# Kernel optimization log

Hardware: AMD Instinct MI355X
Metric: run time of the kernel (lower is better)

Reference implementation:

```python
import math
import jax, jax.numpy as jnp
import numpy as np

SINKHORN_ITERS = 5
SINKHORN_REG = 1.0
D_MODEL, KDIM, VDIM = 512, 512, 512
B, T, N = 8, 2048, 2048


def _xavier(key, shape):
    fan_in, fan_out = shape[0], shape[1]
    bound = math.sqrt(6.0 / (fan_in + fan_out))
    return jax.random.uniform(key, shape, jnp.float32, -bound, bound)


def setup_inputs() -> dict:
    key = jax.random.key(0)
    kq, kk, kv, kQ, kK, kV = jax.random.split(key, 6)
    return {
        "q": jax.random.normal(kq, (T, D_MODEL), jnp.float32),
        "k": jax.random.normal(kk, (B, N, KDIM), jnp.float32),
        "v": jax.random.normal(kv, (B, N, VDIM), jnp.float32),
        "Q": _xavier(kQ, (D_MODEL, D_MODEL)),
        "K": _xavier(kK, (KDIM, D_MODEL)),
        "V": _xavier(kV, (VDIM, D_MODEL)),
    }


def _cdist(q, k):
    # q: [T, d], k: [B, N, d] -> Euclidean distances [B, T, N]
    q2 = jnp.sum(q * q, axis=-1)            # [T]
    k2 = jnp.sum(k * k, axis=-1)            # [B, N]
    qk = jnp.einsum('td,bnd->btn', q, k)    # [B, T, N]
    sq = q2[None, :, None] + k2[:, None, :] - 2.0 * qk
    return jnp.sqrt(jnp.maximum(sq, 0.0))


def _sinkhorn(q, k, iters, reg):
    costs = _cdist(q, k)                    # [B, T, N]
    Kmat = -costs / reg
    num_params = k.shape[1]
    num_tokens = q.shape[0]
    log_a = -jnp.log(jnp.float32(num_params))
    log_b = jnp.float32(0.0)
    u = jnp.zeros((k.shape[0], 1, num_params), Kmat.dtype)
    v = jnp.zeros((k.shape[0], num_tokens, 1), Kmat.dtype)
    for _ in range(iters):
        u = log_a - jax.scipy.special.logsumexp(Kmat + v, axis=1, keepdims=True)
        v = log_b - jax.scipy.special.logsumexp(Kmat + u, axis=2, keepdims=True)
    return jnp.exp(Kmat + u + v)


def reference(q, k, v, Q, K, V):
    qp = q @ Q                               # [T, d_model]
    kp = k @ K                               # [B, N, d_model]
    vp = v @ V                               # [B, N, d_model]
    pi = _sinkhorn(qp, kp, SINKHORN_ITERS, SINKHORN_REG)  # [B, T, N]
    return jnp.einsum('btn,bnd->btd', pi, vp)              # [B, T, d_model]
```

## Files before the change

kernel.cpp:

```cpp
#include <hip/hip_runtime.h>
#include <math.h>

#define TT 2048
#define NP 2048
#define BB 8
#define DD 512

#define LOG_A (-7.6246189861593985f)
#define CC 30.0f
#define E30 1.0686475e13f
#define K0U 5.2180055e9f

typedef __attribute__((ext_vector_type(8))) _Float16 f16x8;
typedef __attribute__((ext_vector_type(4))) _Float16 f16x4;
typedef __attribute__((ext_vector_type(4))) float f32x4;

#define MFMA_F16(a, b, c)  __builtin_amdgcn_mfma_f32_16x16x32_f16((a), (b), (c), 0, 0, 0)

__device__ __forceinline__ float f16u2f(unsigned short u) {
    union { unsigned short s; _Float16 h; } v; v.s = u;
    return (float)v.h;
}

__device__ __forceinline__ void gload16(const void* g, void* l) {
    __builtin_amdgcn_global_load_lds(
        (const __attribute__((address_space(1))) void*)g,
        (__attribute__((address_space(3))) void*)l, 16, 0, 0);
}

__device__ __forceinline__ void frag_step_f16(
    const _Float16* sA, const _Float16* sB,
    int lane, int wm, int wn, f32x4 acc[4][4])
{
    const int sb = (lane >> 4) << 11;
    const int rl = (lane & 15) << 4;
    f16x8 a[4], b[4];
    #pragma unroll
    for (int i = 0; i < 4; ++i) {
        a[i] = *(const f16x8*)((const char*)sA + sb + ((wm + i * 16) << 4) + rl);
        b[i] = *(const f16x8*)((const char*)sB + sb + ((wn + i * 16) << 4) + rl);
    }
    #pragma unroll
    for (int i = 0; i < 4; ++i)
        #pragma unroll
        for (int j = 0; j < 4; ++j)
            acc[i][j] = MFMA_F16(a[i], b[j], acc[i][j]);
}

__device__ __forceinline__ void zero_acc(f32x4 acc[4][4]) {
    #pragma unroll
    for (int i = 0; i < 4; ++i)
        #pragma unroll
        for (int j = 0; j < 4; ++j)
            acc[i][j] = (f32x4){0.f, 0.f, 0.f, 0.f};
}

__device__ __forceinline__ void store_plain(
    float* C, int N, int row0, int col0, int lane, int wm, int wn, f32x4 acc[4][4])
{
    #pragma unroll
    for (int i = 0; i < 4; ++i)
        #pragma unroll
        for (int j = 0; j < 4; ++j) {
            int colg = col0 + wn + j * 16 + (lane & 15);
            int rowb = row0 + wm + i * 16 + ((lane >> 4) << 2);
            #pragma unroll
            for (int r = 0; r < 4; ++r)
                C[(size_t)(rowb + r) * N + colg] = acc[i][j][r];
        }
}

__global__ __launch_bounds__(256) void transpose_f16(
    const float* __restrict__ X, _Float16* __restrict__ oT, int R, int C)
{
    const size_t zoff = (size_t)blockIdx.z * R * C;
    const float* Xb = X + zoff;
    _Float16* ob = oT + zoff;
    __shared__ float t[64][65];
    const int bx = blockIdx.x * 64;
    const int by = blockIdx.y * 64;
    const int tx = threadIdx.x & 63, ty = threadIdx.x >> 6;
    #pragma unroll
    for (int r = ty; r < 64; r += 4)
        t[r][tx] = Xb[(size_t)(by + r) * C + bx + tx];
    __syncthreads();
    #pragma unroll
    for (int r = ty; r < 64; r += 4)
        ob[(size_t)(bx + r) * R + by + tx] = (_Float16)t[tx][r];
}

template<int OUT>
__global__ __launch_bounds__(256) void gemm_proj_f16(
    const float* __restrict__ A, const _Float16* __restrict__ Bt,
    _Float16* __restrict__ C, int M, int N, int K)
{
    __shared__ __attribute__((aligned(16))) _Float16 sA[4096], sB[4096];
    const int tid = threadIdx.x;
    const int lane = tid & 63;
    const int row0 = blockIdx.y * 128;
    const int col0 = blockIdx.x * 128;
    const int wm = ((tid >> 7) & 1) * 64;
    const int wn = ((tid >> 6) & 1) * 64;
    f32x4 acc[4][4];
    zero_acc(acc);

    for (int k0 = 0; k0 < K; k0 += 32) {
        __syncthreads();
        #pragma unroll
        for (int q = 0; q < 2; ++q) {
            int o = (tid + (q << 8)) << 4;
            int s = o >> 11;
            int r = (o & 2047) >> 4;
            gload16(Bt + (size_t)(col0 + r) * K + k0 + s * 8, (char*)sB + o);
            const float* src = A + (size_t)(row0 + r) * K + k0 + s * 8;
            float4 f0 = *(const float4*)src;
            float4 f1 = *(const float4*)(src + 4);
            _Float16 hs[8] = {(_Float16)f0.x, (_Float16)f0.y,
                              (_Float16)f0.z, (_Float16)f0.w,
                              (_Float16)f1.x, (_Float16)f1.y,
                              (_Float16)f1.z, (_Float16)f1.w};
            *(f16x8*)((char*)sA + o) = *(f16x8*)hs;
        }
        __syncthreads();
        frag_step_f16(sA, sB, lane, wm, wn, acc);
    }
    #pragma unroll
    for (int i = 0; i < 4; ++i)
        #pragma unroll
        for (int j = 0; j < 4; ++j) {
            int colg = col0 + wn + j * 16 + (lane & 15);
            int rowb = row0 + wm + i * 16 + ((lane >> 4) << 2);
            if (OUT == 1) {
                #pragma unroll
                for (int r = 0; r < 4; ++r)
                    C[(size_t)(rowb + r) * N + colg] = (_Float16)acc[i][j][r];
            } else {
                int b = rowb >> 11;
                int n0 = rowb & (NP - 1);
                _Float16 h4[4];
                #pragma unroll
                for (int r = 0; r < 4; ++r) h4[r] = (_Float16)acc[i][j][r];
                *(f16x4*)(C + (size_t)b * DD * NP + (size_t)colg * NP + n0) =
                    *(f16x4*)h4;
            }
        }
}

__global__ __launch_bounds__(256) void rownorm_f16(
    const _Float16* __restrict__ X, float* __restrict__ o, int rows)
{
    int w = blockIdx.x * 4 + (threadIdx.x >> 6);
    int lane = threadIdx.x & 63;
    if (w >= rows) return;
    f16x8 v = *(const f16x8*)(X + (size_t)w * DD + lane * 8);
    float s = 0.f;
    #pragma unroll
    for (int j = 0; j < 8; ++j) {
        float x = (float)v[j];
        s = fmaf(x, x, s);
    }
    #pragma unroll
    for (int off = 32; off; off >>= 1) s += __shfl_down(s, off, 64);
    if (lane == 0) o[w] = s;
}

__global__ __launch_bounds__(256) void gemm_cost_f16(
    const _Float16* __restrict__ A, const _Float16* __restrict__ B,
    const float* __restrict__ q2, const float* __restrict__ k2,
    _Float16* __restrict__ E)
{
    const int bid = blockIdx.x;
    const int sid = ((bid & 7) << 8) | (bid >> 3);
    const int b  = sid >> 8;
    const int by = (sid >> 4) & 15;
    const int bx = sid & 15;

    const _Float16* Bb = B + (size_t)b * NP * DD;
    const float* k2b = k2 + (size_t)b * NP;
    _Float16* Cb = E + (size_t)b * TT * NP;

    __shared__ __attribute__((aligned(16))) _Float16 sA[2][4096], sB[2][4096];
    const int tid = threadIdx.x;
    const int lane = tid & 63;
    const int row0 = by * 128;
    const int col0 = bx * 128;
    const int wm = ((tid >> 7) & 1) * 64;
    const int wn = ((tid >> 6) & 1) * 64;
    f32x4 acc[4][4];
    zero_acc(acc);

    auto STAGE = [&](int buf, int k0) {
        #pragma unroll
        for (int q = 0; q < 2; ++q) {
            int o = (tid + (q << 8)) << 4;
            int s = o >> 11;
            int r = (o & 2047) >> 4;
            gload16(A + (size_t)(row0 + r) * DD + k0 + s * 8, (char*)&sA[buf][0] + o);
            gload16(Bb + (size_t)(col0 + r) * DD + k0 + s * 8, (char*)&sB[buf][0] + o);
        }
    };

    STAGE(0, 0);
    __syncthreads();
    int cur = 0;
    for (int k0 = 0; k0 < DD; k0 += 32) {
        if (k0 + 32 < DD) STAGE(cur ^ 1, k0 + 32);
        frag_step_f16(&sA[cur][0], &sB[cur][0], lane, wm, wn, acc);
        __syncthreads();
        cur ^= 1;
    }

    _Float16* half0 = &sA[0][0];
    _Float16* half1 = &sB[0][0];
    #pragma unroll
    for (int i = 0; i < 4; ++i)
        #pragma unroll
        for (int j = 0; j < 4; ++j) {
            int lc = wn + j * 16 + (lane & 15);
            float k2v = k2b[col0 + lc];
            int lrb = wm + i * 16 + ((lane >> 4) << 2);
            #pragma unroll
            for (int r = 0; r < 4; ++r) {
                float sq = q2[row0 + lrb + r] + k2v - 2.f * acc[i][j][r];
                float dist = sqrtf(fmaxf(sq, 0.f));
                float e = fminf(__expf(CC - dist), 60000.f);
                if (wm == 0) half0[(lrb + r) * 128 + lc] = (_Float16)e;
                else         half1[(lrb + r - 64) * 128 + lc] = (_Float16)e;
            }
        }
    __syncthreads();
    {
        const int lr16 = tid >> 4;
        const int c8 = (tid & 15) * 8;
        #pragma unroll
        for (int m = 0; m < 4; ++m) {
            int lr = m * 16 + lr16;
            f16x8 vrow = *(const f16x8*)(half0 + lr * 128 + c8);
            *(f16x8*)(Cb + (size_t)(row0 + lr) * NP + col0 + c8) = vrow;
        }
        #pragma unroll
        for (int m = 0; m < 4; ++m) {
            int lr = 64 + m * 16 + lr16;
            f16x8 vrow = *(const f16x8*)(half1 + (lr - 64) * 128 + c8);
            *(f16x8*)(Cb + (size_t)(row0 + lr) * NP + col0 + c8) = vrow;
        }
    }
}

template<bool FIRST>
__global__ __launch_bounds__(256) void sink_fused(
    const _Float16* __restrict__ E, const float* __restrict__ U,
    float* __restrict__ ps)
{
    const int b = blockIdx.y;
    const int t0 = blockIdx.x * 32;
    const int tid = threadIdx.x;
    const int n0 = tid * 8;
    const _Float16* Eb = E + ((size_t)b * TT + t0) * NP;

    float u8[8];
    if (!FIRST) {
        float4 a = *(const float4*)(U + (size_t)b * NP + n0);
        float4 c = *(const float4*)(U + (size_t)b * NP + n0 + 4);
        u8[0] = a.x; u8[1] = a.y; u8[2] = a.z; u8[3] = a.w;
        u8[4] = c.x; u8[5] = c.y; u8[6] = c.z; u8[7] = c.w;
    }

    float cs[8] = {0.f, 0.f, 0.f, 0.f, 0.f, 0.f, 0.f, 0.f};
    __shared__ float red[8][256];
    __shared__ float yy[8];

    #pragma unroll
    for (int g = 0; g < 4; ++g) {
        uint4 ev[8];
        #pragma unroll
        for (int r = 0; r < 8; ++r)
            ev[r] = *(const uint4*)(Eb + (size_t)(g * 8 + r) * NP + n0);

        if (!FIRST) {
            #pragma unroll
            for (int r = 0; r < 8; ++r) {
                float d = 0.f;
                d = fmaf(f16u2f((unsigned short)(ev[r].x & 0xFFFFu)), u8[0], d);
                d = fmaf(f16u2f((unsigned short)(ev[r].x >> 16)),     u8[1], d);
                d = fmaf(f16u2f((unsigned short)(ev[r].y & 0xFFFFu)), u8[2], d);
                d = fmaf(f16u2f((unsigned short)(ev[r].y >> 16)),     u8[3], d);
                d = fmaf(f16u2f((unsigned short)(ev[r].z & 0xFFFFu)), u8[4], d);
                d = fmaf(f16u2f((unsigned short)(ev[r].z >> 16)),     u8[5], d);
                d = fmaf(f16u2f((unsigned short)(ev[r].w & 0xFFFFu)), u8[6], d);
                d = fmaf(f16u2f((unsigned short)(ev[r].w >> 16)),     u8[7], d);
                red[r][tid] = d;
            }
            __syncthreads();
            {
                int w = tid >> 6, lane = tid & 63;
                #pragma unroll
                for (int rr = 0; rr < 2; ++rr) {
                    int r = w * 2 + rr;
                    float s = red[r][lane] + red[r][lane + 64] +
                              red[r][lane + 128] + red[r][lane + 192];
                    #pragma unroll
                    for (int off = 32; off; off >>= 1)
                        s += __shfl_down(s, off, 64);
                    if (lane == 0) yy[r] = E30 / s;
                }
            }
            __syncthreads();
            #pragma unroll
            for (int r = 0; r < 8; ++r) {
                float yv = yy[r];
                cs[0] = fmaf(f16u2f((unsigned short)(ev[r].x & 0xFFFFu)), yv, cs[0]);
                cs[1] = fmaf(f16u2f((unsigned short)(ev[r].x >> 16)),     yv, cs[1]);
                cs[2] = fmaf(f16u2f((unsigned short)(ev[r].y & 0xFFFFu)), yv, cs[2]);
                cs[3] = fmaf(f16u2f((unsigned short)(ev[r].y >> 16)),     yv, cs[3]);
                cs[4] = fmaf(f16u2f((unsigned short)(ev[r].z & 0xFFFFu)), yv, cs[4]);
                cs[5] = fmaf(f16u2f((unsigned short)(ev[r].z >> 16)),     yv, cs[5]);
                cs[6] = fmaf(f16u2f((unsigned short)(ev[r].w & 0xFFFFu)), yv, cs[6]);
                cs[7] = fmaf(f16u2f((unsigned short)(ev[r].w >> 16)),     yv, cs[7]);
            }
            __syncthreads();
        } else {
            #pragma unroll
            for (int r = 0; r < 8; ++r) {
                cs[0] += f16u2f((unsigned short)(ev[r].x & 0xFFFFu));
                cs[1] += f16u2f((unsigned short)(ev[r].x >> 16));
                cs[2] += f16u2f((unsigned short)(ev[r].y & 0xFFFFu));
                cs[3] += f16u2f((unsigned short)(ev[r].y >> 16));
                cs[4] += f16u2f((unsigned short)(ev[r].z & 0xFFFFu));
                cs[5] += f16u2f((unsigned short)(ev[r].z >> 16));
                cs[6] += f16u2f((unsigned short)(ev[r].w & 0xFFFFu));
                cs[7] += f16u2f((unsigned short)(ev[r].w >> 16));
            }
        }
    }

    size_t o = ((size_t)b * 64 + blockIdx.x) * NP + n0;
    *(float4*)(ps + o)     = make_float4(cs[0], cs[1], cs[2], cs[3]);
    *(float4*)(ps + o + 4) = make_float4(cs[4], cs[5], cs[6], cs[7]);
}

__global__ __launch_bounds__(256) void u_combine(
    const float* __restrict__ ps, float* __restrict__ U)
{
    int gid = blockIdx.x * 256 + threadIdx.x;
    int b = gid >> 11;
    int n = gid & (NP - 1);
    float S = 0.f;
    #pragma unroll 8
    for (int c = 0; c < 64; ++c)
        S += ps[((size_t)b * 64 + c) * NP + n];
    U[gid] = K0U / S;
}

__global__ __launch_bounds__(256) void v_final(
    const _Float16* __restrict__ E, const float* __restrict__ U,
    _Float16* __restrict__ P)
{
    const int b = blockIdx.y;
    const int t = blockIdx.x;
    const uint4* Eb = (const uint4*)(E + ((size_t)b * TT + t) * NP);
    const float* Ub = U + (size_t)b * NP;
    const int tid = threadIdx.x;

    uint4 w = Eb[tid];
    const int n0 = tid * 8;
    float4 u0 = *(const float4*)(Ub + n0);
    float4 u1 = *(const float4*)(Ub + n0 + 4);
    float ev[8];
    ev[0] = f16u2f((unsigned short)(w.x & 0xFFFFu));
    ev[1] = f16u2f((unsigned short)(w.x >> 16));
    ev[2] = f16u2f((unsigned short)(w.y & 0xFFFFu));
    ev[3] = f16u2f((unsigned short)(w.y >> 16));
    ev[4] = f16u2f((unsigned short)(w.z & 0xFFFFu));
    ev[5] = f16u2f((unsigned short)(w.z >> 16));
    ev[6] = f16u2f((unsigned short)(w.w & 0xFFFFu));
    ev[7] = f16u2f((unsigned short)(w.w >> 16));
    float uv[8] = {u0.x, u0.y, u0.z, u0.w, u1.x, u1.y, u1.z, u1.w};

    float s = 0.f;
    #pragma unroll
    for (int j = 0; j < 8; ++j) s = fmaf(ev[j], uv[j], s);
    #pragma unroll
    for (int off = 32; off; off >>= 1) s += __shfl_down(s, off, 64);

    __shared__ float sw[4];
    __shared__ float Sall;
    if ((tid & 63) == 0) sw[tid >> 6] = s;
    __syncthreads();
    if (tid == 0) Sall = sw[0] + sw[1] + sw[2] + sw[3];
    __syncthreads();
    float invS = 1.0f / Sall;
    _Float16 hp[8];
    #pragma unroll
    for (int j = 0; j < 8; ++j)
        hp[j] = (_Float16)(ev[j] * uv[j] * invS);
    *(f16x8*)(P + ((size_t)b * TT + t) * NP + n0) = *(f16x8*)hp;
}

__global__ __launch_bounds__(256) void gemm_pi_f16(
    const _Float16* __restrict__ P, const _Float16* __restrict__ B,
    float* __restrict__ out)
{
    const int bid = blockIdx.x;
    const int sid = ((bid & 7) << 6) | (bid >> 3);
    const int b  = sid >> 6;
    const int by = (sid >> 2) & 15;
    const int bx = sid & 3;

    const _Float16* Pb = P + (size_t)b * TT * NP;
    const _Float16* Bb = B + (size_t)b * DD * NP;
    float* Cb = out + (size_t)b * TT * DD;

    __shared__ __attribute__((aligned(16))) _Float16 sA[2][4096], sB[2][4096];
    const int tid = threadIdx.x;
    const int lane = tid & 63;
    const int row0 = by * 128;
    const int col0 = bx * 128;
    const int wm = ((tid >> 7) & 1) * 64;
    const int wn = ((tid >> 6) & 1) * 64;
    f32x4 acc[4][4];
    zero_acc(acc);

    auto STAGE = [&](int buf, int k0) {
        #pragma unroll
        for (int q = 0; q < 2; ++q) {
            int o = (tid + (q << 8)) << 4;
            int s = o >> 11;
            int r = (o & 2047) >> 4;
            gload16(Pb + (size_t)(row0 + r) * NP + k0 + s * 8, (char*)&sA[buf][0] + o);
            gload16(Bb + (size_t)(col0 + r) * NP + k0 + s * 8, (char*)&sB[buf][0] + o);
        }
    };

    STAGE(0, 0);
    __syncthreads();
    int cur = 0;
    for (int k0 = 0; k0 < NP; k0 += 32) {
        if (k0 + 32 < NP) STAGE(cur ^ 1, k0 + 32);
        frag_step_f16(&sA[cur][0], &sB[cur][0], lane, wm, wn, acc);
        __syncthreads();
        cur ^= 1;
    }
    store_plain(Cb, DD, row0, col0, lane, wm, wn, acc);
}

extern "C" void kernel_launch(void* const* d_in, const int* in_sizes, int n_in,
                              void* d_out, int out_size, void* d_ws, size_t ws_size,
                              hipStream_t stream)
{
    const float* q  = (const float*)d_in[0];
    const float* k  = (const float*)d_in[1];
    const float* v  = (const float*)d_in[2];
    const float* Qw = (const float*)d_in[3];
    const float* Kw = (const float*)d_in[4];
    const float* Vw = (const float*)d_in[5];
    float* out = (float*)d_out;

    char* base = (char*)d_ws;
    _Float16* E16 = (_Float16*)base;
    char* p2 = base + (size_t)BB * TT * NP * 2;
    _Float16* P   = (_Float16*)p2; p2 += (size_t)BB * TT * NP * 2;
    _Float16* qpf = (_Float16*)p2; p2 += (size_t)TT * DD * 2;
    _Float16* kpf = (_Float16*)p2; p2 += (size_t)BB * NP * DD * 2;
    _Float16* vpt = (_Float16*)p2; p2 += (size_t)BB * DD * NP * 2;
    float* q2 = (float*)p2; p2 += (size_t)TT * 4;
    float* k2 = (float*)p2; p2 += (size_t)BB * NP * 4;
    float* U  = (float*)p2; p2 += (size_t)BB * NP * 4;
    float* ps = (float*)p2; p2 += (size_t)BB * 64 * NP * 4;

    _Float16* wq = (_Float16*)base;
    _Float16* wk = wq + 262144;
    _Float16* wv = wk + 262144;

    dim3 blk(256);

    transpose_f16<<<dim3(8, 8, 1), blk, 0, stream>>>(Qw, wq, 512, 512);
    transpose_f16<<<dim3(8, 8, 1), blk, 0, stream>>>(Kw, wk, 512, 512);
    transpose_f16<<<dim3(8, 8, 1), blk, 0, stream>>>(Vw, wv, 512, 512);

    gemm_proj_f16<1><<<dim3(4, 16, 1), blk, 0, stream>>>(q, wq, qpf, TT, DD, DD);
    gemm_proj_f16<1><<<dim3(4, 128, 1), blk, 0, stream>>>(k, wk, kpf, BB * NP, DD, DD);
    gemm_proj_f16<2><<<dim3(4, 128, 1), blk, 0, stream>>>(v, wv, vpt, BB * NP, DD, DD);

    rownorm_f16<<<dim3(TT / 4), blk, 0, stream>>>(qpf, q2, TT);
    rownorm_f16<<<dim3((BB * NP) / 4), blk, 0, stream>>>(kpf, k2, BB * NP);

    gemm_cost_f16<<<dim3(2048), blk, 0, stream>>>(qpf, kpf, q2, k2, E16);

    sink_fused<true><<<dim3(TT / 32, BB), blk, 0, stream>>>(E16, U, ps);
    u_combine<<<dim3(BB * NP / 256), blk, 0, stream>>>(ps, U);
    for (int it = 0; it < 4; ++it) {
        sink_fused<false><<<dim3(TT / 32, BB), blk, 0, stream>>>(E16, U, ps);
        u_combine<<<dim3(BB * NP / 256), blk, 0, stream>>>(ps, U);
    }
    v_final<<<dim3(TT, BB), blk, 0, stream>>>(E16, U, P);

    gemm_pi_f16<<<dim3(512), blk, 0, stream>>>(P, vpt, out);
}
```

Baseline: 424.1 us.

## Triple-buffer cost GEMM, write cost tile directly, merge projection and norm launches

The cost GEMM moves from a double-buffered loop to a three-stage LDS ring. It uses explicit vmcnt waits and raw barriers so that global loads overlap the MFMA steps with fewer full syncs. Its epilogue now writes each f16 exp-cost value straight to global memory instead of staging it through LDS for 16-byte row stores, which may weaken store coalescing. The three weight transposes, the q/k projections and the two row-norm passes are each merged into single launches, relying on q and k buffers being contiguous, to cut launch overhead.

```diff
diff --git a/kernel.cpp b/kernel.cpp
--- a/kernel.cpp
+++ b/kernel.cpp
@@ -70,29 +70,83 @@
         }
 }
 
-__global__ __launch_bounds__(256) void transpose_f16(
-    const float* __restrict__ X, _Float16* __restrict__ oT, int R, int C)
-{
-    const size_t zoff = (size_t)blockIdx.z * R * C;
-    const float* Xb = X + zoff;
-    _Float16* ob = oT + zoff;
+__global__ __launch_bounds__(256) void transpose3_f16(
+    const float* __restrict__ X0, const float* __restrict__ X1,
+    const float* __restrict__ X2, _Float16* __restrict__ o0,
+    _Float16* __restrict__ o1, _Float16* __restrict__ o2)
+{
+    const int z = blockIdx.z;
+    const float* Xb = (z == 0) ? X0 : (z == 1) ? X1 : X2;
+    _Float16* ob = (z == 0) ? o0 : (z == 1) ? o1 : o2;
     __shared__ float t[64][65];
     const int bx = blockIdx.x * 64;
     const int by = blockIdx.y * 64;
     const int tx = threadIdx.x & 63, ty = threadIdx.x >> 6;
     #pragma unroll
     for (int r = ty; r < 64; r += 4)
-        t[r][tx] = Xb[(size_t)(by + r) * C + bx + tx];
+        t[r][tx] = Xb[(size_t)(by + r) * 512 + bx + tx];
     __syncthreads();
     #pragma unroll
     for (int r = ty; r < 64; r += 4)
-        ob[(size_t)(bx + r) * R + by + tx] = (_Float16)t[tx][r];
-}
-
-template<int OUT>
-__global__ __launch_bounds__(256) void gemm_proj_f16(
+        ob[(size_t)(bx + r) * 512 + by + tx] = (_Float16)t[tx][r];
+}
+
+__global__ __launch_bounds__(256) void gemm_projqk_f16(
+    const float* __restrict__ Aq, const float* __restrict__ Ak,
+    const _Float16* __restrict__ Btq, const _Float16* __restrict__ Btk,
+    _Float16* __restrict__ C)
+{
+    const int by = blockIdx.y;
+    const bool isq = (by < 16);
+    const float* A = isq ? Aq : Ak;
+    const _Float16* Bt = isq ? Btq : Btk;
+    const int arow0 = isq ? by * 128 : (by - 16) * 128;
+    const int crow0 = by * 128;
+    const int col0 = blockIdx.x * 128;
+
+    __shared__ __attribute__((aligned(16))) _Float16 sA[4096], sB[4096];
+    const int tid = threadIdx.x;
+    const int lane = tid & 63;
+    const int wm = ((tid >> 7) & 1) * 64;
+    const int wn = ((tid >> 6) & 1) * 64;
+    f32x4 acc[4][4];
+    zero_acc(acc);
+
+    for (int k0 = 0; k0 < DD; k0 += 32) {
+        __syncthreads();
+        #pragma unroll
+        for (int q = 0; q < 2; ++q) {
+            int o = (tid + (q << 8)) << 4;
+            int s = o >> 11;
+            int r = (o & 2047) >> 4;
+            gload16(Bt + (size_t)(col0 + r) * DD + k0 + s * 8, (char*)sB + o);
+            const float* src = A + (size_t)(arow0 + r) * DD + k0 + s * 8;
+            float4 f0 = *(const float4*)src;
+            float4 f1 = *(const float4*)(src + 4);
+            _Float16 hs[8] = {(_Float16)f0.x, (_Float16)f0.y,
+                              (_Float16)f0.z, (_Float16)f0.w,
+                              (_Float16)f1.x, (_Float16)f1.y,
+                              (_Float16)f1.z, (_Float16)f1.w};
+            *(f16x8*)((char*)sA + o) = *(f16x8*)hs;
+        }
+        __syncthreads();
+        frag_step_f16(sA, sB, lane, wm, wn, acc);
+    }
+    #pragma unroll
+    for (int i = 0; i < 4; ++i)
+        #pragma unroll
+        for (int j = 0; j < 4; ++j) {
+            int colg = col0 + wn + j * 16 + (lane & 15);
+            int rowb = crow0 + wm + i * 16 + ((lane >> 4) << 2);
+            #pragma unroll
+            for (int r = 0; r < 4; ++r)
+                C[(size_t)(rowb + r) * DD + colg] = (_Float16)acc[i][j][r];
+        }
+}
+
+__global__ __launch_bounds__(256) void gemm_projv_f16(
     const float* __restrict__ A, const _Float16* __restrict__ Bt,
-    _Float16* __restrict__ C, int M, int N, int K)
+    _Float16* __restrict__ C)
 {
     __shared__ __attribute__((aligned(16))) _Float16 sA[4096], sB[4096];
     const int tid = threadIdx.x;
@@ -104,15 +158,15 @@
     f32x4 acc[4][4];
     zero_acc(acc);
 
-    for (int k0 = 0; k0 < K; k0 += 32) {
+    for (int k0 = 0; k0 < DD; k0 += 32) {
         __syncthreads();
         #pragma unroll
         for (int q = 0; q < 2; ++q) {
             int o = (tid + (q << 8)) << 4;
             int s = o >> 11;
             int r = (o & 2047) >> 4;
-            gload16(Bt + (size_t)(col0 + r) * K + k0 + s * 8, (char*)sB + o);
-            const float* src = A + (size_t)(row0 + r) * K + k0 + s * 8;
+            gload16(Bt + (size_t)(col0 + r) * DD + k0 + s * 8, (char*)sB + o);
+            const float* src = A + (size_t)(row0 + r) * DD + k0 + s * 8;
             float4 f0 = *(const float4*)src;
             float4 f1 = *(const float4*)(src + 4);
             _Float16 hs[8] = {(_Float16)f0.x, (_Float16)f0.y,
@@ -130,19 +184,13 @@
         for (int j = 0; j < 4; ++j) {
             int colg = col0 + wn + j * 16 + (lane & 15);
             int rowb = row0 + wm + i * 16 + ((lane >> 4) << 2);
-            if (OUT == 1) {
-                #pragma unroll
-                for (int r = 0; r < 4; ++r)
-                    C[(size_t)(rowb + r) * N + colg] = (_Float16)acc[i][j][r];
-            } else {
-                int b = rowb >> 11;
-                int n0 = rowb & (NP - 1);
-                _Float16 h4[4];
-                #pragma unroll
-                for (int r = 0; r < 4; ++r) h4[r] = (_Float16)acc[i][j][r];
-                *(f16x4*)(C + (size_t)b * DD * NP + (size_t)colg * NP + n0) =
-                    *(f16x4*)h4;
-            }
+            int b = rowb >> 11;
+            int n0 = rowb & (NP - 1);
+            _Float16 h4[4];
+            #pragma unroll
+            for (int r = 0; r < 4; ++r) h4[r] = (_Float16)acc[i][j][r];
+            *(f16x4*)(C + (size_t)b * DD * NP + (size_t)colg * NP + n0) =
+                *(f16x4*)h4;
         }
 }
 
@@ -179,7 +227,7 @@
     const float* k2b = k2 + (size_t)b * NP;
     _Float16* Cb = E + (size_t)b * TT * NP;
 
-    __shared__ __attribute__((aligned(16))) _Float16 sA[2][4096], sB[2][4096];
+    __shared__ __attribute__((aligned(16))) _Float16 sA[3][4096], sB[3][4096];
     const int tid = threadIdx.x;
     const int lane = tid & 63;
     const int row0 = by * 128;
@@ -201,50 +249,40 @@
     };
 
     STAGE(0, 0);
-    __syncthreads();
-    int cur = 0;
-    for (int k0 = 0; k0 < DD; k0 += 32) {
-        if (k0 + 32 < DD) STAGE(cur ^ 1, k0 + 32);
-        frag_step_f16(&sA[cur][0], &sB[cur][0], lane, wm, wn, acc);
-        __syncthreads();
-        cur ^= 1;
-    }
-
-    _Float16* half0 = &sA[0][0];
-    _Float16* half1 = &sB[0][0];
+    STAGE(1, 32);
+
+    #pragma unroll
+    for (int s = 0; s < 14; ++s) {
+        asm volatile("s_waitcnt vmcnt(4)" ::: "memory");
+        __builtin_amdgcn_s_barrier();
+        __builtin_amdgcn_sched_barrier(0);
+        STAGE((s + 2) % 3, (s + 2) * 32);
+        frag_step_f16(&sA[s % 3][0], &sB[s % 3][0], lane, wm, wn, acc);
+    }
+    asm volatile("s_waitcnt vmcnt(4)" ::: "memory");
+    __builtin_amdgcn_s_barrier();
+    __builtin_amdgcn_sched_barrier(0);
+    frag_step_f16(&sA[2][0], &sB[2][0], lane, wm, wn, acc);
+    asm volatile("s_waitcnt vmcnt(0)" ::: "memory");
+    __builtin_amdgcn_s_barrier();
+    __builtin_amdgcn_sched_barrier(0);
+    frag_step_f16(&sA[0][0], &sB[0][0], lane, wm, wn, acc);
+
     #pragma unroll
     for (int i = 0; i < 4; ++i)
         #pragma unroll
         for (int j = 0; j < 4; ++j) {
-            int lc = wn + j * 16 + (lane & 15);
-            float k2v = k2b[col0 + lc];
-            int lrb = wm + i * 16 + ((lane >> 4) << 2);
+            int colg = col0 + wn + j * 16 + (lane & 15);
+            float k2v = k2b[colg];
+            int rowb = row0 + wm + i * 16 + ((lane >> 4) << 2);
             #pragma unroll
             for (int r = 0; r < 4; ++r) {
-                float sq = q2[row0 + lrb + r] + k2v - 2.f * acc[i][j][r];
+                float sq = q2[rowb + r] + k2v - 2.f * acc[i][j][r];
                 float dist = sqrtf(fmaxf(sq, 0.f));
                 float e = fminf(__expf(CC - dist), 60000.f);
-                if (wm == 0) half0[(lrb + r) * 128 + lc] = (_Float16)e;
-                else         half1[(lrb + r - 64) * 128 + lc] = (_Float16)e;
+                Cb[(size_t)(rowb + r) * NP + colg] = (_Float16)e;
             }
         }
-    __syncthreads();
-    {
-        const int lr16 = tid >> 4;
-        const int c8 = (tid & 15) * 8;
-        #pragma unroll
-        for (int m = 0; m < 4; ++m) {
-            int lr = m * 16 + lr16;
-            f16x8 vrow = *(const f16x8*)(half0 + lr * 128 + c8);
-            *(f16x8*)(Cb + (size_t)(row0 + lr) * NP + col0 + c8) = vrow;
-        }
-        #pragma unroll
-        for (int m = 0; m < 4; ++m) {
-            int lr = 64 + m * 16 + lr16;
-            f16x8 vrow = *(const f16x8*)(half1 + (lr - 64) * 128 + c8);
-            *(f16x8*)(Cb + (size_t)(row0 + lr) * NP + col0 + c8) = vrow;
-        }
-    }
 }
 
 template<bool FIRST>
@@ -474,16 +512,12 @@
 
     dim3 blk(256);
 
-    transpose_f16<<<dim3(8, 8, 1), blk, 0, stream>>>(Qw, wq, 512, 512);
-    transpose_f16<<<dim3(8, 8, 1), blk, 0, stream>>>(Kw, wk, 512, 512);
-    transpose_f16<<<dim3(8, 8, 1), blk, 0, stream>>>(Vw, wv, 512, 512);
-
-    gemm_proj_f16<1><<<dim3(4, 16, 1), blk, 0, stream>>>(q, wq, qpf, TT, DD, DD);
-    gemm_proj_f16<1><<<dim3(4, 128, 1), blk, 0, stream>>>(k, wk, kpf, BB * NP, DD, DD);
-    gemm_proj_f16<2><<<dim3(4, 128, 1), blk, 0, stream>>>(v, wv, vpt, BB * NP, DD, DD);
-
-    rownorm_f16<<<dim3(TT / 4), blk, 0, stream>>>(qpf, q2, TT);
-    rownorm_f16<<<dim3((BB * NP) / 4), blk, 0, stream>>>(kpf, k2, BB * NP);
+    transpose3_f16<<<dim3(8, 8, 3), blk, 0, stream>>>(Qw, Kw, Vw, wq, wk, wv);
+
+    gemm_projqk_f16<<<dim3(4, 144, 1), blk, 0, stream>>>(q, k, wq, wk, qpf);
+    gemm_projv_f16<<<dim3(4, 128, 1), blk, 0, stream>>>(v, wv, vpt);
+
+    rownorm_f16<<<dim3((TT + BB * NP) / 4), blk, 0, stream>>>(qpf, q2, TT + BB * NP);
 
     gemm_cost_f16<<<dim3(2048), blk, 0, stream>>>(qpf, kpf, q2, k2, E16);
 
```

Result: faster. 392.5 us (-7.5%).
